# Performance work log

Hardware: AMD Instinct MI355X
Metric: run time of the kernel (lower is better)

Reference implementation:

```python
import jax, jax.numpy as jnp
import numpy as np

N_NODES = 100000
N_EDGES = 1600000
DIM = 128


def setup_inputs() -> dict:
    key = jax.random.key(0)
    k1, k2, k3, k4 = jax.random.split(key, 4)
    x = jax.random.normal(k1, (N_NODES, DIM), dtype=jnp.float32)
    edge_index = jax.random.randint(k2, (2, N_EDGES), 0, N_NODES, dtype=jnp.int64)
    scale = 1.0 / np.sqrt(DIM)
    W1 = jax.random.normal(k3, (DIM, DIM), dtype=jnp.float32) * scale
    W2 = jax.random.normal(k4, (DIM, DIM), dtype=jnp.float32) * scale
    b1 = jnp.zeros((DIM,), dtype=jnp.float32)
    b2 = jnp.zeros((DIM,), dtype=jnp.float32)
    return {"x": x, "edge_index": edge_index, "W1": W1, "b1": b1, "W2": W2, "b2": b2}


def _gcn_conv(x, src, dst, dinv, W, b, n):
    # linear transform first (PyG GCNConv), then normalized scatter-add aggregation
    h = x @ W                                   # [N, out]
    norm = dinv[src] * dinv[dst]                # [E+N]
    msg = h[src] * norm[:, None]                # [E+N, out]
    agg = jax.ops.segment_sum(msg, dst, num_segments=n)
    return agg + b


def reference(x, edge_index, W1, b1, W2, b2):
    n = x.shape[0]
    loops = jnp.arange(n, dtype=edge_index.dtype)
    src = jnp.concatenate([edge_index[0], loops])  # add self-loops
    dst = jnp.concatenate([edge_index[1], loops])
    deg = jax.ops.segment_sum(jnp.ones_like(src, dtype=x.dtype), dst, num_segments=n)
    dinv = jnp.where(deg > 0, jax.lax.rsqrt(deg), 0.0)  # D^{-1/2}
    h = _gcn_conv(x, src, dst, dinv, W1, b1, n)
    h = jax.nn.relu(h)
    out = _gcn_conv(h, src, dst, dinv, W2, b2, n)
    return out
```

## Files before the change

### kernel.cpp

```cpp
#include <hip/hip_runtime.h>
#include <hip/hip_bf16.h>
#include <hip/hip_fp16.h>

#define NN 100000
#define DIM 128
#define NB 391
#define BCAP 5120
#define GTILES ((NN + 63) / 64)

typedef _Float16 f16x8 __attribute__((ext_vector_type(8)));
typedef float f32x4 __attribute__((ext_vector_type(4)));

__global__ void k_zero(int* __restrict__ p, int n) {
    int i = blockIdx.x * blockDim.x + threadIdx.x;
    if (i < n) p[i] = 0;
}

__global__ void k_binA(const int* __restrict__ src, const int* __restrict__ dst,
                       int* __restrict__ bcur, int* __restrict__ binbuf, int E) {
    __shared__ int hist[NB];
    __shared__ int base[NB];
    const int t = threadIdx.x;
    for (int b = t; b < NB; b += 256) hist[b] = 0;
    __syncthreads();

    const int e0 = blockIdx.x * 4096;
    int mys[16], myd[16];
#pragma unroll
    for (int i = 0; i < 16; ++i) {
        const int e = e0 + i * 256 + t;
        int d = -1, s = 0;
        if (e < E) {
            d = dst[e];
            s = src[e];
            atomicAdd(&hist[d >> 8], 1);
        }
        mys[i] = s;
        myd[i] = d;
    }
    __syncthreads();

    for (int b = t; b < NB; b += 256) {
        const int h = hist[b];
        base[b] = h ? atomicAdd(&bcur[b], h) : 0;
    }
    __syncthreads();
    for (int b = t; b < NB; b += 256) hist[b] = 0;
    __syncthreads();

#pragma unroll
    for (int i = 0; i < 16; ++i) {
        const int d = myd[i];
        if (d >= 0) {
            const int b = d >> 8;
            const int loc = atomicAdd(&hist[b], 1);
            const int p = base[b] + loc;
            if (p < BCAP) binbuf[b * BCAP + p] = mys[i] | ((d & 255) << 17);
        }
    }
}

__global__ void k_binCount(const int* __restrict__ bcur, const int* __restrict__ binbuf,
                           int* __restrict__ degi, float* __restrict__ dinv,
                           int* __restrict__ bsum) {
    __shared__ int cnt[256];
    __shared__ int red[256];
    const int b = blockIdx.x;
    const int t = threadIdx.x;
    cnt[t] = 0;
    __syncthreads();
    const int n = min(bcur[b], BCAP);
    const int* p = &binbuf[b * BCAP];
    for (int i = t; i < n; i += 256) atomicAdd(&cnt[p[i] >> 17], 1);
    __syncthreads();
    const int node = b * 256 + t;
    const int c = cnt[t];
    if (node < NN) {
        degi[node] = c;
        dinv[node] = rsqrtf((float)(c + 1));
    }
    red[t] = (node < NN) ? c : 0;
    __syncthreads();
    for (int d = 128; d > 0; d >>= 1) {
        if (t < d) red[t] += red[t + d];
        __syncthreads();
    }
    if (t == 0) bsum[b] = red[0];
}

__global__ void k_scan2(int* __restrict__ bsum, int nb) {
    __shared__ int s[1024];
    const int t = threadIdx.x;
    const int v = (t < nb) ? bsum[t] : 0;
    s[t] = v;
    __syncthreads();
    int acc = v;
    for (int d = 1; d < 1024; d <<= 1) {
        const int o = (t >= d) ? s[t - d] : 0;
        __syncthreads();
        acc += o;
        s[t] = acc;
        __syncthreads();
    }
    if (t < nb) bsum[t] = acc - v;
}

__global__ void k_gemm1(const float* __restrict__ inF, const float* __restrict__ W,
                        const float* __restrict__ dinv, _Float16* __restrict__ outH,
                        const int* __restrict__ degi, const int* __restrict__ bsum,
                        int* __restrict__ rowptr, const int* __restrict__ bcur,
                        const int* __restrict__ binbuf, int* __restrict__ csr) {
    __shared__ int s[256];
    __shared__ int cur[256];
    const int t = threadIdx.x;

    if (blockIdx.x < NB) {
        const int b = blockIdx.x;
        const int node = b * 256 + t;
        const int deg = (node < NN) ? degi[node] : 0;
        s[t] = deg;
        __syncthreads();
        int acc = deg;
        for (int d = 1; d < 256; d <<= 1) {
            const int o = (t >= d) ? s[t - d] : 0;
            __syncthreads();
            acc += o;
            s[t] = acc;
            __syncthreads();
        }
        const int ex = acc - deg + bsum[b];
        cur[t] = ex;
        if (node < NN) {
            rowptr[node] = ex;
            if (node == NN - 1) rowptr[NN] = ex + deg;
        }
        __syncthreads();
        const int n = min(bcur[b], BCAP);
        const int* p = &binbuf[b * BCAP];
        for (int i = t; i < n; i += 256) {
            const int v = p[i];
            const int pos = atomicAdd(&cur[v >> 17], 1);
            csr[pos] = v & 0x1FFFF;
        }
        return;
    }

    const int tile = blockIdx.x - NB;
    const int row0 = tile * 64;
    const int wv   = t >> 6;
    const int l    = t & 63;
    const int l15  = l & 15;
    const int lk8  = (l >> 4) << 3;
    const int colw = wv << 5;

    f16x8 bf[2][4];
#pragma unroll
    for (int ct = 0; ct < 2; ++ct)
#pragma unroll
        for (int kt = 0; kt < 4; ++kt) {
            const int nn = colw + ct * 16 + l15;
            const int k0 = kt * 32 + lk8;
            f16x8 v;
#pragma unroll
            for (int j = 0; j < 8; ++j) v[j] = (_Float16)W[(k0 + j) * DIM + nn];
            bf[ct][kt] = v;
        }

    f32x4 acc[4][2];
#pragma unroll
    for (int rt = 0; rt < 4; ++rt)
#pragma unroll
        for (int ct = 0; ct < 2; ++ct) acc[rt][ct] = (f32x4){0.f, 0.f, 0.f, 0.f};

#pragma unroll
    for (int rt = 0; rt < 4; ++rt) {
        int row = row0 + rt * 16 + l15;
        row = min(row, NN - 1);
        f16x8 a[4];
#pragma unroll
        for (int kt = 0; kt < 4; ++kt) {
            const int k0 = kt * 32 + lk8;
            const float4 v0 = *(const float4*)&inF[row * DIM + k0];
            const float4 v1 = *(const float4*)&inF[row * DIM + k0 + 4];
            f16x8 v;
            v[0] = (_Float16)v0.x; v[1] = (_Float16)v0.y;
            v[2] = (_Float16)v0.z; v[3] = (_Float16)v0.w;
            v[4] = (_Float16)v1.x; v[5] = (_Float16)v1.y;
            v[6] = (_Float16)v1.z; v[7] = (_Float16)v1.w;
            a[kt] = v;
        }
#pragma unroll
        for (int ct = 0; ct < 2; ++ct)
#pragma unroll
            for (int kt = 0; kt < 4; ++kt)
                acc[rt][ct] = __builtin_amdgcn_mfma_f32_16x16x32_f16(a[kt], bf[ct][kt],
                                                                    acc[rt][ct], 0, 0, 0);
    }

#pragma unroll
    for (int rt = 0; rt < 4; ++rt)
#pragma unroll
        for (int r = 0; r < 4; ++r) {
            const int row = row0 + rt * 16 + ((l >> 4) << 2) + r;
            if (row < NN) {
                const float d = dinv[row];
                outH[row * DIM + colw + l15]      = (_Float16)(acc[rt][0][r] * d);
                outH[row * DIM + colw + 16 + l15] = (_Float16)(acc[rt][1][r] * d);
            }
        }
}

__global__ void k_gather_gemm(const __half* __restrict__ hs, const float* __restrict__ W,
                              const float* __restrict__ dinv, const float* __restrict__ b1,
                              _Float16* __restrict__ outH, const int* __restrict__ csr,
                              const int* __restrict__ rowptr) {
    __shared__ _Float16 As[64][136];
    const int t    = threadIdx.x;
    const int wv   = t >> 6;
    const int l    = t & 63;
    const int off  = l << 1;
    const int row0 = blockIdx.x * 64;

    const float2 bb = {b1[off], b1[off + 1]};

#pragma unroll 1
    for (int i = 0; i < 16; ++i) {
        const int lr = wv * 16 + i;
        const int n  = row0 + lr;
        float2 r = {0.f, 0.f};
        if (n < NN) {
            const int start = __builtin_amdgcn_readfirstlane(rowptr[n]);
            const int end   = __builtin_amdgcn_readfirstlane(rowptr[n + 1]);
            float2 a0 = __half22float2(*(const __half2*)&hs[n * DIM + off]);
            float2 a1 = {0.f, 0.f}, a2 = {0.f, 0.f}, a3 = {0.f, 0.f};
            int j = start;
            for (; j + 3 < end; j += 4) {
                const int s0 = __builtin_amdgcn_readfirstlane(csr[j]);
                const int s1 = __builtin_amdgcn_readfirstlane(csr[j + 1]);
                const int s2 = __builtin_amdgcn_readfirstlane(csr[j + 2]);
                const int s3 = __builtin_amdgcn_readfirstlane(csr[j + 3]);
                const float2 v0 = __half22float2(*(const __half2*)&hs[s0 * DIM + off]);
                const float2 v1 = __half22float2(*(const __half2*)&hs[s1 * DIM + off]);
                const float2 v2 = __half22float2(*(const __half2*)&hs[s2 * DIM + off]);
                const float2 v3 = __half22float2(*(const __half2*)&hs[s3 * DIM + off]);
                a0.x += v0.x; a0.y += v0.y;
                a1.x += v1.x; a1.y += v1.y;
                a2.x += v2.x; a2.y += v2.y;
                a3.x += v3.x; a3.y += v3.y;
            }
            for (; j < end; ++j) {
                const int s0 = __builtin_amdgcn_readfirstlane(csr[j]);
                const float2 v0 = __half22float2(*(const __half2*)&hs[s0 * DIM + off]);
                a0.x += v0.x; a0.y += v0.y;
            }
            const float dn = dinv[n];
            r.x = fmaxf(fmaf(dn, a0.x + a1.x + a2.x + a3.x, bb.x), 0.f);
            r.y = fmaxf(fmaf(dn, a0.y + a1.y + a2.y + a3.y, bb.y), 0.f);
        }
        *(__half2*)&As[lr][off] = __floats2half2_rn(r.x, r.y);
    }
    __syncthreads();

    const int l15  = l & 15;
    const int lk8  = (l >> 4) << 3;
    const int colw = wv << 5;

    f16x8 bf[2][4];
#pragma unroll
    for (int ct = 0; ct < 2; ++ct)
#pragma unroll
        for (int kt = 0; kt < 4; ++kt) {
            const int nn = colw + ct * 16 + l15;
            const int k0 = kt * 32 + lk8;
            f16x8 v;
#pragma unroll
            for (int j = 0; j < 8; ++j) v[j] = (_Float16)W[(k0 + j) * DIM + nn];
            bf[ct][kt] = v;
        }

    f32x4 acc[4][2];
#pragma unroll
    for (int rt = 0; rt < 4; ++rt)
#pragma unroll
        for (int ct = 0; ct < 2; ++ct) acc[rt][ct] = (f32x4){0.f, 0.f, 0.f, 0.f};

#pragma unroll
    for (int rt = 0; rt < 4; ++rt) {
        f16x8 a[4];
#pragma unroll
        for (int kt = 0; kt < 4; ++kt)
            a[kt] = *(const f16x8*)&As[rt * 16 + l15][kt * 32 + lk8];
#pragma unroll
        for (int ct = 0; ct < 2; ++ct)
#pragma unroll
            for (int kt = 0; kt < 4; ++kt)
                acc[rt][ct] = __builtin_amdgcn_mfma_f32_16x16x32_f16(a[kt], bf[ct][kt],
                                                                    acc[rt][ct], 0, 0, 0);
    }

#pragma unroll
    for (int rt = 0; rt < 4; ++rt)
#pragma unroll
        for (int r = 0; r < 4; ++r) {
            const int row = row0 + rt * 16 + ((l >> 4) << 2) + r;
            if (row < NN) {
                const float d = dinv[row];
                outH[row * DIM + colw + l15]      = (_Float16)(acc[rt][0][r] * d);
                outH[row * DIM + colw + 16 + l15] = (_Float16)(acc[rt][1][r] * d);
            }
        }
}

__global__ void k_gather2(const __half* __restrict__ hs, float* __restrict__ outF,
                          const int* __restrict__ csr, const int* __restrict__ rowptr,
                          const float* __restrict__ dinv, const float* __restrict__ b2) {
    const int w = (blockIdx.x * blockDim.x + threadIdx.x) >> 6;
    if (w >= NN) return;
    const int lane = threadIdx.x & 63;
    const int off  = lane << 1;

    const int start = __builtin_amdgcn_readfirstlane(rowptr[w]);
    const int end   = __builtin_amdgcn_readfirstlane(rowptr[w + 1]);

    float2 a0 = __half22float2(*(const __half2*)&hs[w * DIM + off]);
    float2 a1 = {0.f, 0.f}, a2 = {0.f, 0.f}, a3 = {0.f, 0.f};

    int j = start;
    for (; j + 3 < end; j += 4) {
        const int s0 = __builtin_amdgcn_readfirstlane(csr[j]);
        const int s1 = __builtin_amdgcn_readfirstlane(csr[j + 1]);
        const int s2 = __builtin_amdgcn_readfirstlane(csr[j + 2]);
        const int s3 = __builtin_amdgcn_readfirstlane(csr[j + 3]);
        const float2 v0 = __half22float2(*(const __half2*)&hs[s0 * DIM + off]);
        const float2 v1 = __half22float2(*(const __half2*)&hs[s1 * DIM + off]);
        const float2 v2 = __half22float2(*(const __half2*)&hs[s2 * DIM + off]);
        const float2 v3 = __half22float2(*(const __half2*)&hs[s3 * DIM + off]);
        a0.x += v0.x; a0.y += v0.y;
        a1.x += v1.x; a1.y += v1.y;
        a2.x += v2.x; a2.y += v2.y;
        a3.x += v3.x; a3.y += v3.y;
    }
    for (; j < end; ++j) {
        const int s0 = __builtin_amdgcn_readfirstlane(csr[j]);
        const float2 v0 = __half22float2(*(const __half2*)&hs[s0 * DIM + off]);
        a0.x += v0.x; a0.y += v0.y;
    }

    const float d = dinv[w];
    const float2 b = *(const float2*)&b2[off];
    float2 r;
    r.x = fmaf(d, a0.x + a1.x + a2.x + a3.x, b.x);
    r.y = fmaf(d, a0.y + a1.y + a2.y + a3.y, b.y);
    *(float2*)&outF[w * DIM + off] = r;
}

extern "C" void kernel_launch(void* const* d_in, const int* in_sizes, int n_in,
                              void* d_out, int out_size, void* d_ws, size_t ws_size,
                              hipStream_t stream) {
    const float* x  = (const float*)d_in[0];
    const int*   ei = (const int*)d_in[1];
    const float* W1 = (const float*)d_in[2];
    const float* b1 = (const float*)d_in[3];
    const float* W2 = (const float*)d_in[4];
    const float* b2 = (const float*)d_in[5];
    float* out = (float*)d_out;

    const int E = in_sizes[1] / 2;
    const int* src = ei;
    const int* dst = ei + E;

    char* ws = (char*)d_ws;
    float*    dinv   = (float*)(ws);
    int*      degi   = (int*)  (ws + (1  << 20));
    int*      rowptr = (int*)  (ws + (2  << 20));
    int*      bsum   = (int*)  (ws + (3  << 20));
    int*      bcur   = (int*)  (ws + (3  << 20) + 65536);
    int*      csr    = (int*)  (ws + (4  << 20));
    int*      binbuf = (int*)  (ws + (11 << 20));
    _Float16* hs     = (_Float16*)(ws + (20 << 20));
    _Float16* hs2    = (_Float16*)(ws + (47 << 20));

    const int ABLK = (E + 4095) / 4096;

    k_zero    <<<(NB + 255) / 256, 256, 0, stream>>>(bcur, NB);
    k_binA    <<<ABLK, 256, 0, stream>>>(src, dst, bcur, binbuf, E);
    k_binCount<<<NB, 256, 0, stream>>>(bcur, binbuf, degi, dinv, bsum);
    k_scan2   <<<1, 1024, 0, stream>>>(bsum, NB);

    k_gemm1<<<NB + GTILES, 256, 0, stream>>>(x, W1, dinv, hs, degi, bsum,
                                             rowptr, bcur, binbuf, csr);

    k_gather_gemm<<<GTILES, 256, 0, stream>>>((const __half*)hs, W2, dinv, b1, hs2,
                                              csr, rowptr);

    k_gather2<<<(NN * 64) / 256, 256, 0, stream>>>((const __half*)hs2, out, csr, rowptr,
                                                   dinv, b2);
}
```

Measured before the change: 256.0 us.

## Store features in 16-column segments and gather per segment with blockIdx-interleaved seg

GEMM outputs are now written in a segmented layout: eight slabs, each holding 16 columns for every node, so a gathered row is 32 bytes and sits in its own smaller working set. Aggregation is split into eight segment passes, with consecutive blocks covering different segments of the same node chunk, and 8 lanes handling each node. This is meant to improve cache hit rates on the random neighbor gathers. The fused gather+GEMM is split into a separate gather kernel and a GEMM that reads from global memory, which adds a round trip through an intermediate fp16 buffer and another launch.

```diff
diff --git a/kernel.cpp b/kernel.cpp
--- a/kernel.cpp
+++ b/kernel.cpp
@@ -7,6 +7,7 @@
 #define NB 391
 #define BCAP 5120
 #define GTILES ((NN + 63) / 64)
+#define SEGN (NN * 16)
 
 typedef _Float16 f16x8 __attribute__((ext_vector_type(8)));
 typedef float f32x4 __attribute__((ext_vector_type(4)));
@@ -204,63 +205,18 @@
             const int row = row0 + rt * 16 + ((l >> 4) << 2) + r;
             if (row < NN) {
                 const float d = dinv[row];
-                outH[row * DIM + colw + l15]      = (_Float16)(acc[rt][0][r] * d);
-                outH[row * DIM + colw + 16 + l15] = (_Float16)(acc[rt][1][r] * d);
+                outH[(2 * wv + 0) * SEGN + row * 16 + l15] = (_Float16)(acc[rt][0][r] * d);
+                outH[(2 * wv + 1) * SEGN + row * 16 + l15] = (_Float16)(acc[rt][1][r] * d);
             }
         }
 }
 
-__global__ void k_gather_gemm(const __half* __restrict__ hs, const float* __restrict__ W,
-                              const float* __restrict__ dinv, const float* __restrict__ b1,
-                              _Float16* __restrict__ outH, const int* __restrict__ csr,
-                              const int* __restrict__ rowptr) {
-    __shared__ _Float16 As[64][136];
-    const int t    = threadIdx.x;
+__global__ void k_gemm2(const _Float16* __restrict__ inH, const float* __restrict__ W,
+                        const float* __restrict__ dinv, _Float16* __restrict__ outH) {
+    const int t = threadIdx.x;
+    const int row0 = blockIdx.x * 64;
     const int wv   = t >> 6;
     const int l    = t & 63;
-    const int off  = l << 1;
-    const int row0 = blockIdx.x * 64;
-
-    const float2 bb = {b1[off], b1[off + 1]};
-
-#pragma unroll 1
-    for (int i = 0; i < 16; ++i) {
-        const int lr = wv * 16 + i;
-        const int n  = row0 + lr;
-        float2 r = {0.f, 0.f};
-        if (n < NN) {
-            const int start = __builtin_amdgcn_readfirstlane(rowptr[n]);
-            const int end   = __builtin_amdgcn_readfirstlane(rowptr[n + 1]);
-            float2 a0 = __half22float2(*(const __half2*)&hs[n * DIM + off]);
-            float2 a1 = {0.f, 0.f}, a2 = {0.f, 0.f}, a3 = {0.f, 0.f};
-            int j = start;
-            for (; j + 3 < end; j += 4) {
-                const int s0 = __builtin_amdgcn_readfirstlane(csr[j]);
-                const int s1 = __builtin_amdgcn_readfirstlane(csr[j + 1]);
-                const int s2 = __builtin_amdgcn_readfirstlane(csr[j + 2]);
-                const int s3 = __builtin_amdgcn_readfirstlane(csr[j + 3]);
-                const float2 v0 = __half22float2(*(const __half2*)&hs[s0 * DIM + off]);
-                const float2 v1 = __half22float2(*(const __half2*)&hs[s1 * DIM + off]);
-                const float2 v2 = __half22float2(*(const __half2*)&hs[s2 * DIM + off]);
-                const float2 v3 = __half22float2(*(const __half2*)&hs[s3 * DIM + off]);
-                a0.x += v0.x; a0.y += v0.y;
-                a1.x += v1.x; a1.y += v1.y;
-                a2.x += v2.x; a2.y += v2.y;
-                a3.x += v3.x; a3.y += v3.y;
-            }
-            for (; j < end; ++j) {
-                const int s0 = __builtin_amdgcn_readfirstlane(csr[j]);
-                const float2 v0 = __half22float2(*(const __half2*)&hs[s0 * DIM + off]);
-                a0.x += v0.x; a0.y += v0.y;
-            }
-            const float dn = dinv[n];
-            r.x = fmaxf(fmaf(dn, a0.x + a1.x + a2.x + a3.x, bb.x), 0.f);
-            r.y = fmaxf(fmaf(dn, a0.y + a1.y + a2.y + a3.y, bb.y), 0.f);
-        }
-        *(__half2*)&As[lr][off] = __floats2half2_rn(r.x, r.y);
-    }
-    __syncthreads();
-
     const int l15  = l & 15;
     const int lk8  = (l >> 4) << 3;
     const int colw = wv << 5;
@@ -286,10 +242,12 @@
 
 #pragma unroll
     for (int rt = 0; rt < 4; ++rt) {
+        int row = row0 + rt * 16 + l15;
+        row = min(row, NN - 1);
         f16x8 a[4];
 #pragma unroll
         for (int kt = 0; kt < 4; ++kt)
-            a[kt] = *(const f16x8*)&As[rt * 16 + l15][kt * 32 + lk8];
+            a[kt] = *(const f16x8*)&inH[row * DIM + kt * 32 + lk8];
 #pragma unroll
         for (int ct = 0; ct < 2; ++ct)
 #pragma unroll
@@ -305,53 +263,63 @@
             const int row = row0 + rt * 16 + ((l >> 4) << 2) + r;
             if (row < NN) {
                 const float d = dinv[row];
-                outH[row * DIM + colw + l15]      = (_Float16)(acc[rt][0][r] * d);
-                outH[row * DIM + colw + 16 + l15] = (_Float16)(acc[rt][1][r] * d);
+                outH[(2 * wv + 0) * SEGN + row * 16 + l15] = (_Float16)(acc[rt][0][r] * d);
+                outH[(2 * wv + 1) * SEGN + row * 16 + l15] = (_Float16)(acc[rt][1][r] * d);
             }
         }
 }
 
-__global__ void k_gather2(const __half* __restrict__ hs, float* __restrict__ outF,
-                          const int* __restrict__ csr, const int* __restrict__ rowptr,
-                          const float* __restrict__ dinv, const float* __restrict__ b2) {
-    const int w = (blockIdx.x * blockDim.x + threadIdx.x) >> 6;
-    if (w >= NN) return;
-    const int lane = threadIdx.x & 63;
-    const int off  = lane << 1;
-
-    const int start = __builtin_amdgcn_readfirstlane(rowptr[w]);
-    const int end   = __builtin_amdgcn_readfirstlane(rowptr[w + 1]);
-
-    float2 a0 = __half22float2(*(const __half2*)&hs[w * DIM + off]);
-    float2 a1 = {0.f, 0.f}, a2 = {0.f, 0.f}, a3 = {0.f, 0.f};
+template <int FINAL>
+__global__ void k_gather_seg(const _Float16* __restrict__ hsSeg, _Float16* __restrict__ aggH,
+                             float* __restrict__ outF, const int* __restrict__ csr,
+                             const int* __restrict__ rowptr, const float* __restrict__ dinv,
+                             const float* __restrict__ bias) {
+    const int seg   = blockIdx.x & 7;
+    const int chunk = blockIdx.x >> 3;
+    const int t     = threadIdx.x;
+    const int wv    = t >> 6;
+    const int lane  = t & 63;
+    const int grp   = lane >> 3;
+    const int gl    = lane & 7;
+    const int n     = chunk * 32 + wv * 8 + grp;
+
+    const _Float16* __restrict__ hp = hsSeg + seg * SEGN;
+    const int col = seg * 16 + (gl << 1);
+
+    const int start = rowptr[n];
+    const int end   = rowptr[n + 1];
+
+    float2 a0 = __half22float2(*(const __half2*)&hp[n * 16 + (gl << 1)]);
+    float2 a1 = {0.f, 0.f};
 
     int j = start;
-    for (; j + 3 < end; j += 4) {
-        const int s0 = __builtin_amdgcn_readfirstlane(csr[j]);
-        const int s1 = __builtin_amdgcn_readfirstlane(csr[j + 1]);
-        const int s2 = __builtin_amdgcn_readfirstlane(csr[j + 2]);
-        const int s3 = __builtin_amdgcn_readfirstlane(csr[j + 3]);
-        const float2 v0 = __half22float2(*(const __half2*)&hs[s0 * DIM + off]);
-        const float2 v1 = __half22float2(*(const __half2*)&hs[s1 * DIM + off]);
-        const float2 v2 = __half22float2(*(const __half2*)&hs[s2 * DIM + off]);
-        const float2 v3 = __half22float2(*(const __half2*)&hs[s3 * DIM + off]);
+    for (; j + 1 < end; j += 2) {
+        const int s0 = csr[j];
+        const int s1 = csr[j + 1];
+        const float2 v0 = __half22float2(*(const __half2*)&hp[s0 * 16 + (gl << 1)]);
+        const float2 v1 = __half22float2(*(const __half2*)&hp[s1 * 16 + (gl << 1)]);
         a0.x += v0.x; a0.y += v0.y;
         a1.x += v1.x; a1.y += v1.y;
-        a2.x += v2.x; a2.y += v2.y;
-        a3.x += v3.x; a3.y += v3.y;
-    }
-    for (; j < end; ++j) {
-        const int s0 = __builtin_amdgcn_readfirstlane(csr[j]);
-        const float2 v0 = __half22float2(*(const __half2*)&hs[s0 * DIM + off]);
+    }
+    if (j < end) {
+        const int s0 = csr[j];
+        const float2 v0 = __half22float2(*(const __half2*)&hp[s0 * 16 + (gl << 1)]);
         a0.x += v0.x; a0.y += v0.y;
     }
 
-    const float d = dinv[w];
-    const float2 b = *(const float2*)&b2[off];
-    float2 r;
-    r.x = fmaf(d, a0.x + a1.x + a2.x + a3.x, b.x);
-    r.y = fmaf(d, a0.y + a1.y + a2.y + a3.y, b.y);
-    *(float2*)&outF[w * DIM + off] = r;
+    const float dn = dinv[n];
+    const float2 bb = {bias[col], bias[col + 1]};
+    if constexpr (FINAL) {
+        float2 r;
+        r.x = fmaf(dn, a0.x + a1.x, bb.x);
+        r.y = fmaf(dn, a0.y + a1.y, bb.y);
+        *(float2*)&outF[n * DIM + col] = r;
+    } else {
+        float2 r;
+        r.x = fmaxf(fmaf(dn, a0.x + a1.x, bb.x), 0.f);
+        r.y = fmaxf(fmaf(dn, a0.y + a1.y, bb.y), 0.f);
+        *(__half2*)&aggH[n * DIM + col] = __floats2half2_rn(r.x, r.y);
+    }
 }
 
 extern "C" void kernel_launch(void* const* d_in, const int* in_sizes, int n_in,
@@ -379,6 +347,7 @@
     int*      binbuf = (int*)  (ws + (11 << 20));
     _Float16* hs     = (_Float16*)(ws + (20 << 20));
     _Float16* hs2    = (_Float16*)(ws + (47 << 20));
+    _Float16* aggH   = (_Float16*)(ws + (74 << 20));
 
     const int ABLK = (E + 4095) / 4096;
 
@@ -389,10 +358,10 @@
 
     k_gemm1<<<NB + GTILES, 256, 0, stream>>>(x, W1, dinv, hs, degi, bsum,
                                              rowptr, bcur, binbuf, csr);
-
-    k_gather_gemm<<<GTILES, 256, 0, stream>>>((const __half*)hs, W2, dinv, b1, hs2,
-                                              csr, rowptr);
-
-    k_gather2<<<(NN * 64) / 256, 256, 0, stream>>>((const __half*)hs2, out, csr, rowptr,
-                                                   dinv, b2);
-}
+    k_gather_seg<0><<<(NN / 32) * 8, 256, 0, stream>>>(hs, aggH, nullptr, csr, rowptr,
+                                                       dinv, b1);
+
+    k_gemm2<<<GTILES, 256, 0, stream>>>(aggH, W2, dinv, hs2);
+    k_gather_seg<1><<<(NN / 32) * 8, 256, 0, stream>>>(hs2, nullptr, out, csr, rowptr,
+                                                       dinv, b2);
+}
```

Result: slower. 337.0 us (+31.7%).
